# Kernel tuning notes

Hardware: AMD Instinct MI355X
Metric: run time of the kernel (lower is better)

Reference implementation:

```python
import jax, jax.numpy as jnp
import numpy as np

NEG_SLOPE = 0.2


def _gat_layer(x, src, dst, W, att_s, att_d, bias):
    # x: [N, F_in]; W: [F_in, H*C]; att_s/att_d: [H, C]; bias: [H*C]
    N = x.shape[0]
    H, C = att_s.shape
    h = (x @ W).reshape(N, H, C)                      # projected features [N,H,C]
    a_src = jnp.einsum('nhc,hc->nh', h, att_s)        # [N,H] per-node src logits
    a_dst = jnp.einsum('nhc,hc->nh', h, att_d)        # [N,H]
    e = a_src[src] + a_dst[dst]                       # [E,H] edge logits
    e = jnp.where(e > 0, e, NEG_SLOPE * e)            # leaky_relu
    # scatter-softmax over incoming edges of each destination node
    m = jax.ops.segment_max(e, dst, num_segments=N)   # [N,H]
    ex = jnp.exp(e - m[dst])                          # [E,H]
    denom = jax.ops.segment_sum(ex, dst, num_segments=N)  # [N,H]
    alpha = ex / denom[dst]                           # [E,H]
    # scatter-add aggregation of weighted source features
    msg = h[src] * alpha[:, :, None]                  # [E,H,C]
    out = jax.ops.segment_sum(msg, dst, num_segments=N)   # [N,H,C]
    return out.reshape(N, H * C) + bias


def _with_self_loops(edge_index, N):
    loop = jnp.arange(N, dtype=edge_index.dtype)
    src = jnp.concatenate([edge_index[0], loop])
    dst = jnp.concatenate([edge_index[1], loop])
    return src, dst


def setup_inputs() -> dict:
    key = jax.random.key(0)
    ks = jax.random.split(key, 10)
    N, E = 50000, 800000
    F_in, C1, H1, F_out = 128, 64, 4, 128
    x = jax.random.normal(ks[0], (N, F_in), dtype=jnp.float32)
    edge_index = jax.random.randint(ks[1], (2, E), 0, N, dtype=jnp.int64)
    s1 = 1.0 / np.sqrt(F_in)
    W1 = jax.random.normal(ks[2], (F_in, H1 * C1), dtype=jnp.float32) * s1
    att_src1 = jax.random.normal(ks[3], (H1, C1), dtype=jnp.float32) * 0.1
    att_dst1 = jax.random.normal(ks[4], (H1, C1), dtype=jnp.float32) * 0.1
    bias1 = jnp.zeros((H1 * C1,), dtype=jnp.float32)
    s2 = 1.0 / np.sqrt(H1 * C1)
    W2 = jax.random.normal(ks[5], (H1 * C1, F_out), dtype=jnp.float32) * s2
    att_src2 = jax.random.normal(ks[6], (1, F_out), dtype=jnp.float32) * 0.1
    att_dst2 = jax.random.normal(ks[7], (1, F_out), dtype=jnp.float32) * 0.1
    bias2 = jnp.zeros((F_out,), dtype=jnp.float32)
    return {"x": x, "edge_index": edge_index,
            "W1": W1, "att_src1": att_src1, "att_dst1": att_dst1, "bias1": bias1,
            "W2": W2, "att_src2": att_src2, "att_dst2": att_dst2, "bias2": bias2}


def reference(x, edge_index, W1, att_src1, att_dst1, bias1,
              W2, att_src2, att_dst2, bias2):
    N = x.shape[0]
    src, dst = _with_self_loops(edge_index, N)
    h1 = _gat_layer(x, src, dst, W1, att_src1, att_dst1, bias1)
    h1 = jax.nn.elu(h1)
    out = _gat_layer(h1, src, dst, W2, att_src2, att_dst2, bias2)
    return out
```

## Files before the change

kernel.cpp:

```cpp
#include <hip/hip_runtime.h>

#define NN 50000
#define NE 800000

constexpr int H1 = 4, F1 = 128, HC1 = 256;
constexpr int HC2 = 128;

typedef unsigned short u16;
typedef unsigned int u32;
typedef __attribute__((ext_vector_type(8))) short bf16x8;
typedef __attribute__((ext_vector_type(4))) float f32x4;

__device__ __forceinline__ float bf2f(u16 h) {
    return __uint_as_float(((u32)h) << 16);
}
__device__ __forceinline__ u16 f2bf(float f) {
    u32 u = __float_as_uint(f);
    u32 r = (u + 0x7fffu + ((u >> 16) & 1u)) >> 16;
    return (u16)r;
}

__device__ __forceinline__ int ld_edge(const int* e32, const long long* e64, int is64, long long idx) {
    return is64 ? (int)e64[idx] : e32[idx];
}

__global__ __launch_bounds__(256) void k_prep(
    const float* __restrict__ x, const float* __restrict__ W1, const float* __restrict__ W2,
    const float* __restrict__ as1w, const float* __restrict__ ad1w,
    const float* __restrict__ as2w, const float* __restrict__ ad2w,
    u16* __restrict__ xb, u16* __restrict__ wp1, u16* __restrict__ wp2,
    float* __restrict__ wa1, float* __restrict__ wa2)
{
    const int b = blockIdx.x, tid = threadIdx.x;
    if (b < 3125) {
        int i = b * 256 + tid;
        const float4* p = (const float4*)x + (size_t)i * 2;
        float4 a = p[0], c = p[1];
        ushort4 o0, o1;
        o0.x = f2bf(a.x); o0.y = f2bf(a.y); o0.z = f2bf(a.z); o0.w = f2bf(a.w);
        o1.x = f2bf(c.x); o1.y = f2bf(c.y); o1.z = f2bf(c.z); o1.w = f2bf(c.w);
        ((ushort4*)xb)[(size_t)i * 2] = o0;
        ((ushort4*)xb)[(size_t)i * 2 + 1] = o1;
    } else if (b < 3253) {
        int o = (b - 3125) * 256 + tid;
        int j = o & 7, lk = (o >> 3) & 3, nn = (o >> 5) & 255, kc = o >> 13;
        int k = kc * 32 + lk * 8 + j;
        wp1[o] = f2bf(W1[(size_t)k * HC1 + nn]);
    } else if (b < 3381) {
        int o = (b - 3253) * 256 + tid;
        int j = o & 7, lk = (o >> 3) & 3, nn = (o >> 5) & 127, kc = o >> 12;
        int k = kc * 32 + lk * 8 + j;
        wp2[o] = f2bf(W2[(size_t)k * HC2 + nn]);
    } else {
        #pragma unroll
        for (int pp = 0; pp < 2; pp++) {
            int p = tid + pp * 256;
            int k = p >> 2, h = p & 3;
            float s = 0.f, d = 0.f;
            for (int c = 0; c < 64; c++) {
                float wv = W1[(size_t)k * HC1 + h * 64 + c];
                s = fmaf(wv, as1w[h * 64 + c], s);
                d = fmaf(wv, ad1w[h * 64 + c], d);
            }
            wa1[h * 128 + k] = s;
            wa1[(4 + h) * 128 + k] = d;
        }
        {
            int k = tid;
            float s = 0.f, d = 0.f;
            for (int c = 0; c < 128; c++) {
                float wv = W2[(size_t)k * HC2 + c];
                s = fmaf(wv, as2w[c], s);
                d = fmaf(wv, ad2w[c], d);
            }
            wa2[k * 2] = s;
            wa2[k * 2 + 1] = d;
        }
    }
}

__global__ void k_zero_detect(int* __restrict__ p, const int* __restrict__ e32, int* __restrict__ flag) {
    int i = blockIdx.x * blockDim.x + threadIdx.x;
    if (i < NN) p[i] = 1;
    if (i == 0) {
        int z = 1;
        for (int t = 0; t < 16; t++)
            if (e32[2 * t + 1] != 0) z = 0;
        *flag = z;
    }
}

__global__ void k_count(const int* __restrict__ e32, const long long* __restrict__ e64,
                        const int* __restrict__ flag, int* __restrict__ deg) {
    int e = blockIdx.x * blockDim.x + threadIdx.x;
    if (e >= NE) return;
    int is64 = *flag;
    int dst = ld_edge(e32, e64, is64, (long long)NE + e);
    atomicAdd(&deg[dst], 1);
}

__global__ __launch_bounds__(256) void k_part(const int* __restrict__ deg, int* __restrict__ bsum) {
    int i = blockIdx.x * 256 + threadIdx.x;
    int v = (i < NN) ? deg[i] : 0;
    #pragma unroll
    for (int off = 1; off < 64; off <<= 1) v += __shfl_xor(v, off);
    __shared__ int ws[4];
    if ((threadIdx.x & 63) == 0) ws[threadIdx.x >> 6] = v;
    __syncthreads();
    if (threadIdx.x == 0) bsum[blockIdx.x] = ws[0] + ws[1] + ws[2] + ws[3];
}

__global__ __launch_bounds__(256) void k_scanb(const int* __restrict__ bsum, int* __restrict__ boff,
                                               int* __restrict__ row_ptr, int NB) {
    const int tid = threadIdx.x;
    const int lane = tid & 63, wv = tid >> 6;
    int v = (tid < NB) ? bsum[tid] : 0;
    int x = v;
    #pragma unroll
    for (int off = 1; off < 64; off <<= 1) {
        int t = __shfl_up(x, off);
        if (lane >= off) x += t;
    }
    __shared__ int wsum[4], woff[4];
    if (lane == 63) wsum[wv] = x;
    __syncthreads();
    if (tid == 0) {
        int run = 0;
        #pragma unroll
        for (int j = 0; j < 4; j++) { woff[j] = run; run += wsum[j]; }
        row_ptr[NN] = run;
    }
    __syncthreads();
    if (tid < NB) boff[tid] = x - v + woff[wv];
}

__global__ __launch_bounds__(256) void k_addb(const int* __restrict__ deg, const int* __restrict__ boff,
                                              int* __restrict__ row_ptr, int* __restrict__ cursor,
                                              int* __restrict__ col) {
    const int tid = threadIdx.x;
    const int lane = tid & 63, wv = tid >> 6;
    int i = blockIdx.x * 256 + tid;
    int v = (i < NN) ? deg[i] : 0;
    int x = v;
    #pragma unroll
    for (int off = 1; off < 64; off <<= 1) {
        int t = __shfl_up(x, off);
        if (lane >= off) x += t;
    }
    __shared__ int wsum[4], woff[4];
    if (lane == 63) wsum[wv] = x;
    __syncthreads();
    if (tid == 0) {
        int run = 0;
        #pragma unroll
        for (int j = 0; j < 4; j++) { woff[j] = run; run += wsum[j]; }
    }
    __syncthreads();
    int excl = x - v + woff[wv] + boff[blockIdx.x];
    if (i < NN) {
        row_ptr[i] = excl;
        cursor[i] = excl + 1;
        col[excl] = i;
    }
}

__global__ void k_fill(const int* __restrict__ e32, const long long* __restrict__ e64,
                       const int* __restrict__ flag, int* __restrict__ cursor, int* __restrict__ col) {
    int e = blockIdx.x * blockDim.x + threadIdx.x;
    if (e >= NE) return;
    int is64 = *flag;
    int src = ld_edge(e32, e64, is64, e);
    int dst = ld_edge(e32, e64, is64, (long long)NE + e);
    int pos = atomicAdd(&cursor[dst], 1);
    col[pos] = src;
}

template <int K, int NOUT, int TPB>
__global__ __launch_bounds__(TPB) void k_gemm_mfma(
    const u16* __restrict__ Ab, const u16* __restrict__ Wp, u16* __restrict__ Hout, int M)
{
    constexpr int BM = 64, BK = 32;
    constexpr int NK = K / BK;
    constexpr int LDA = 40;
    __shared__ __align__(16) u16 As[2][BM * LDA];

    const int tid = threadIdx.x;
    const int w = tid >> 6;
    const int l = tid & 63;
    const int l15 = l & 15, lk = l >> 4;
    const int row0 = blockIdx.x * BM;
    const int col0 = w * 64;

    f32x4 acc[4][4];
    #pragma unroll
    for (int rt = 0; rt < 4; rt++)
        #pragma unroll
        for (int nt = 0; nt < 4; nt++)
            acc[rt][nt] = (f32x4){0.f, 0.f, 0.f, 0.f};

    auto stage = [&](int kc, int b) {
        #pragma unroll
        for (int i = tid; i < BM * 4; i += TPB) {
            int r = i >> 2, c = (i & 3) * 8;
            int gr = row0 + r;
            bf16x8 v = {0, 0, 0, 0, 0, 0, 0, 0};
            if (gr < M) v = *(const bf16x8*)(Ab + (size_t)gr * K + kc * BK + c);
            *(bf16x8*)&As[b][r * LDA + c] = v;
        }
    };
    auto loadB = [&](int kc, bf16x8* bf) {
        #pragma unroll
        for (int nt = 0; nt < 4; nt++)
            bf[nt] = *(const bf16x8*)(Wp + (((size_t)kc * NOUT + col0 + nt * 16 + l15) * 4 + lk) * 8);
    };

    bf16x8 bcur[4];
    loadB(0, bcur);
    stage(0, 0);
    for (int kc = 0; kc < NK; ++kc) {
        __syncthreads();
        bf16x8 afr[4];
        #pragma unroll
        for (int rt = 0; rt < 4; rt++)
            afr[rt] = *(const bf16x8*)&As[kc & 1][(rt * 16 + l15) * LDA + lk * 8];
        bf16x8 bnext[4];
        if (kc + 1 < NK) {
            loadB(kc + 1, bnext);
            stage(kc + 1, (kc + 1) & 1);
        }
        #pragma unroll
        for (int rt = 0; rt < 4; rt++)
            #pragma unroll
            for (int nt = 0; nt < 4; nt++)
                acc[rt][nt] = __builtin_amdgcn_mfma_f32_16x16x32_bf16(afr[rt], bcur[nt], acc[rt][nt], 0, 0, 0);
        if (kc + 1 < NK) {
            #pragma unroll
            for (int nt = 0; nt < 4; nt++) bcur[nt] = bnext[nt];
        }
    }

    #pragma unroll
    for (int rt = 0; rt < 4; rt++) {
        #pragma unroll
        for (int t = 0; t < 4; t++) {
            int gr = row0 + rt * 16 + lk * 4 + t;
            if (gr < M) {
                #pragma unroll
                for (int nt = 0; nt < 4; nt++)
                    Hout[(size_t)gr * NOUT + col0 + nt * 16 + l15] = f2bf(acc[rt][nt][t]);
            }
        }
    }
}

__global__ __launch_bounds__(256) void k_logits1(
    const u16* __restrict__ xb, const float* __restrict__ wa1,
    float* __restrict__ as1, float* __restrict__ ad1)
{
    __shared__ float wsm[8 * 128];
    for (int i = threadIdx.x; i < 1024; i += 256) wsm[i] = wa1[i];
    __syncthreads();
    int n = blockIdx.x * 4 + (threadIdx.x >> 6);
    int l = threadIdx.x & 63;
    u32 xx = *(const u32*)(xb + (size_t)n * F1 + l * 2);
    float x0 = bf2f((u16)(xx & 0xffff)), x1 = bf2f((u16)(xx >> 16));
    float a[8];
    #pragma unroll
    for (int j = 0; j < 8; j++)
        a[j] = x0 * wsm[j * 128 + l * 2] + x1 * wsm[j * 128 + l * 2 + 1];
    #pragma unroll
    for (int off = 1; off < 64; off <<= 1) {
        #pragma unroll
        for (int j = 0; j < 8; j++) a[j] += __shfl_xor(a[j], off);
    }
    if (l == 0) {
        *(float4*)(as1 + (size_t)n * 4) = make_float4(a[0], a[1], a[2], a[3]);
        *(float4*)(ad1 + (size_t)n * 4) = make_float4(a[4], a[5], a[6], a[7]);
    }
}

__global__ __launch_bounds__(256) void k_agg1(
    const int* __restrict__ row_ptr, const int* __restrict__ col,
    const u16* __restrict__ Hb, const float* __restrict__ as_, const float* __restrict__ ad_,
    const float* __restrict__ bias, const float* __restrict__ wa2,
    u16* __restrict__ outp, float* __restrict__ as2, float* __restrict__ ad2)
{
    __shared__ int    s_src[4][64];
    __shared__ float4 s_p[4][64];
    int n = blockIdx.x * 4 + (threadIdx.x >> 6);
    const int lane = threadIdx.x & 63;
    const int wv = threadIdx.x >> 6;
    const int head = lane >> 4;
    float4 ad4 = *(const float4*)(ad_ + (size_t)n * 4);
    int beg = row_ptr[n];
    int cnt = row_ptr[n + 1] - beg;
    float4 sp = make_float4(0.f, 0.f, 0.f, 0.f);
    float ax = 0.f, ay = 0.f, az = 0.f, aw = 0.f;
    for (int c = 0; c < cnt; c += 64) {
        int idx = c + lane;
        int srcl = 0;
        float4 p4 = make_float4(0.f, 0.f, 0.f, 0.f);
        if (idx < cnt) {
            srcl = __builtin_nontemporal_load(col + beg + idx);
            float4 a4 = *(const float4*)(as_ + (size_t)srcl * 4);
            float e;
            e = a4.x + ad4.x; e = e > 0.f ? e : 0.2f * e; p4.x = __expf(e);
            e = a4.y + ad4.y; e = e > 0.f ? e : 0.2f * e; p4.y = __expf(e);
            e = a4.z + ad4.z; e = e > 0.f ? e : 0.2f * e; p4.z = __expf(e);
            e = a4.w + ad4.w; e = e > 0.f ? e : 0.2f * e; p4.w = __expf(e);
        }
        sp.x += p4.x; sp.y += p4.y; sp.z += p4.z; sp.w += p4.w;
        s_src[wv][lane] = srcl;
        s_p[wv][lane] = p4;
        int jmax = min(64, cnt - c);
        #pragma unroll 4
        for (int j = 0; j < jmax; ++j) {
            int srcj = s_src[wv][j];
            float pj = ((const float*)&s_p[wv][j])[head];
            ushort4 hv = *(const ushort4*)(Hb + (size_t)srcj * HC1 + lane * 4);
            ax = fmaf(pj, bf2f(hv.x), ax);
            ay = fmaf(pj, bf2f(hv.y), ay);
            az = fmaf(pj, bf2f(hv.z), az);
            aw = fmaf(pj, bf2f(hv.w), aw);
        }
    }
    #pragma unroll
    for (int off = 1; off < 64; off <<= 1) {
        sp.x += __shfl_xor(sp.x, off);
        sp.y += __shfl_xor(sp.y, off);
        sp.z += __shfl_xor(sp.z, off);
        sp.w += __shfl_xor(sp.w, off);
    }
    float s = head < 2 ? (head == 0 ? sp.x : sp.y) : (head == 2 ? sp.z : sp.w);
    float inv = 1.f / s;
    float4 bv = *(const float4*)(bias + lane * 4);
    float4 o;
    o.x = ax * inv + bv.x;
    o.y = ay * inv + bv.y;
    o.z = az * inv + bv.z;
    o.w = aw * inv + bv.w;
    o.x = o.x > 0.f ? o.x : __expf(o.x) - 1.f;
    o.y = o.y > 0.f ? o.y : __expf(o.y) - 1.f;
    o.z = o.z > 0.f ? o.z : __expf(o.z) - 1.f;
    o.w = o.w > 0.f ? o.w : __expf(o.w) - 1.f;
    ushort4 ob;
    ob.x = f2bf(o.x); ob.y = f2bf(o.y); ob.z = f2bf(o.z); ob.w = f2bf(o.w);
    *(ushort4*)(outp + (size_t)n * HC1 + lane * 4) = ob;

    float4 wA = *(const float4*)(wa2 + lane * 8);
    float4 wB = *(const float4*)(wa2 + lane * 8 + 4);
    float s2 = o.x * wA.x + o.y * wA.z + o.z * wB.x + o.w * wB.z;
    float d2 = o.x * wA.y + o.y * wA.w + o.z * wB.y + o.w * wB.w;
    #pragma unroll
    for (int off = 1; off < 64; off <<= 1) {
        s2 += __shfl_xor(s2, off);
        d2 += __shfl_xor(d2, off);
    }
    if (lane == 0) { as2[n] = s2; ad2[n] = d2; }
}

__global__ __launch_bounds__(256) void k_agg2(
    const int* __restrict__ row_ptr, const int* __restrict__ col,
    const u16* __restrict__ Hb, const float* __restrict__ as_, const float* __restrict__ ad_,
    const float* __restrict__ bias, float* __restrict__ outp)
{
    __shared__ int   s_src[4][64];
    __shared__ float s_p[4][64];
    int n = blockIdx.x * 4 + (threadIdx.x >> 6);
    const int lane = threadIdx.x & 63;
    const int wv = threadIdx.x >> 6;
    float ad0 = ad_[n];
    int beg = row_ptr[n];
    int cnt = row_ptr[n + 1] - beg;
    float sp = 0.f;
    float ax = 0.f, ay = 0.f;
    for (int c = 0; c < cnt; c += 64) {
        int idx = c + lane;
        int srcl = 0;
        float p = 0.f;
        if (idx < cnt) {
            srcl = __builtin_nontemporal_load(col + beg + idx);
            float e = as_[srcl] + ad0;
            e = e > 0.f ? e : 0.2f * e;
            p = __expf(e);
        }
        sp += p;
        s_src[wv][lane] = srcl;
        s_p[wv][lane] = p;
        int jmax = min(64, cnt - c);
        #pragma unroll 4
        for (int j = 0; j < jmax; ++j) {
            int srcj = s_src[wv][j];
            float pj = s_p[wv][j];
            ushort2 hv = *(const ushort2*)(Hb + (size_t)srcj * HC2 + lane * 2);
            ax = fmaf(pj, bf2f(hv.x), ax);
            ay = fmaf(pj, bf2f(hv.y), ay);
        }
    }
    #pragma unroll
    for (int off = 1; off < 64; off <<= 1) sp += __shfl_xor(sp, off);
    float inv = 1.f / sp;
    float2 bv = *(const float2*)(bias + lane * 2);
    float2 o = make_float2(ax * inv + bv.x, ay * inv + bv.y);
    *(float2*)(outp + (size_t)n * HC2 + lane * 2) = o;
}

extern "C" void kernel_launch(void* const* d_in, const int* in_sizes, int n_in,
                              void* d_out, int out_size, void* d_ws, size_t ws_size,
                              hipStream_t stream) {
    const float* x   = (const float*)d_in[0];
    const int*       e32 = (const int*)d_in[1];
    const long long* e64 = (const long long*)d_in[1];
    const float* W1  = (const float*)d_in[2];
    const float* as1w = (const float*)d_in[3];
    const float* ad1w = (const float*)d_in[4];
    const float* b1  = (const float*)d_in[5];
    const float* W2  = (const float*)d_in[6];
    const float* as2w = (const float*)d_in[7];
    const float* ad2w = (const float*)d_in[8];
    const float* b2  = (const float*)d_in[9];
    float* out = (float*)d_out;

    char* w = (char*)d_ws;
    auto carve = [&](size_t bytes) -> void* {
        void* p = (void*)w;
        w += (bytes + 255) & ~(size_t)255;
        return p;
    };
    int*   flag    = (int*)carve(4);
    int*   row_ptr = (int*)carve((NN + 1) * sizeof(int));
    int*   cursor  = (int*)carve(NN * sizeof(int));
    int*   col     = (int*)carve((NE + NN) * sizeof(int));
    int*   bsum    = (int*)carve(256 * sizeof(int));
    int*   boff    = (int*)carve(256 * sizeof(int));
    float* as1     = (float*)carve((size_t)NN * H1 * sizeof(float));
    float* ad1     = (float*)carve((size_t)NN * H1 * sizeof(float));
    float* as2     = (float*)carve((size_t)NN * sizeof(float));
    float* ad2     = (float*)carve((size_t)NN * sizeof(float));
    u16*   xb      = (u16*)carve((size_t)NN * F1 * sizeof(u16));
    u16*   h1b     = (u16*)carve((size_t)NN * HC1 * sizeof(u16));
    u16*   h2in    = (u16*)carve((size_t)NN * HC1 * sizeof(u16));
    u16*   h2b     = (u16*)carve((size_t)NN * HC2 * sizeof(u16));
    u16*   wp1     = (u16*)carve((size_t)F1 * HC1 * sizeof(u16));
    u16*   wp2     = (u16*)carve((size_t)HC1 * HC2 * sizeof(u16));
    float* wa1     = (float*)carve(8 * 128 * sizeof(float));
    float* wa2     = (float*)carve(256 * 2 * sizeof(float));

    const int TPB = 256;
    const int gN  = (NN + TPB - 1) / TPB;
    const int gE  = (NE + TPB - 1) / TPB;
    const int gM  = (NN + 63) / 64;
    const int gAgg = NN / 4;

    k_prep<<<3382, 256, 0, stream>>>(x, W1, W2, as1w, ad1w, as2w, ad2w, xb, wp1, wp2, wa1, wa2);

    k_zero_detect<<<gN, TPB, 0, stream>>>(cursor, e32, flag);
    k_count<<<gE, TPB, 0, stream>>>(e32, e64, flag, cursor);
    k_part<<<gN, TPB, 0, stream>>>(cursor, bsum);
    k_scanb<<<1, 256, 0, stream>>>(bsum, boff, row_ptr, gN);
    k_addb<<<gN, TPB, 0, stream>>>(cursor, boff, row_ptr, cursor, col);
    k_fill<<<gE, TPB, 0, stream>>>(e32, e64, flag, cursor, col);

    k_gemm_mfma<F1, HC1, 256><<<gM, 256, 0, stream>>>(xb, wp1, h1b, NN);
    k_logits1<<<gAgg, 256, 0, stream>>>(xb, wa1, as1, ad1);
    k_agg1<<<gAgg, TPB, 0, stream>>>(row_ptr, col, h1b, as1, ad1, b1, wa2, h2in, as2, ad2);

    k_gemm_mfma<HC1, HC2, 128><<<gM, 128, 0, stream>>>(h2in, wp2, h2b, NN);
    k_agg2<<<gAgg, TPB, 0, stream>>>(row_ptr, col, h2b, as2, ad2, b2, out);
}
```

Measured before the change: 276.0 us.

## Slice feature tables into 32-channel column blocks and split aggregation across slices

The GEMM now writes projected features in a sliced layout (32-channel slabs, node-major within each slab). Edge softmax weights are precomputed per edge into a buffer by a separate kernel, and aggregation is split into per-slice blocks. In each block, 8 lanes cover 32 channels and 8 edges are processed in parallel, then reduced with shuffles. The aim is to shrink the random-gather working set per block so it stays cache resident and to raise parallelism per destination node. The cost is extra kernel launches, an extra edge-weight buffer written and read, and col/row_ptr being reread once per slice.

```diff
diff --git a/kernel.cpp b/kernel.cpp
--- a/kernel.cpp
+++ b/kernel.cpp
@@ -2,6 +2,7 @@
 
 #define NN 50000
 #define NE 800000
+#define NEA (NE + NN)
 
 constexpr int H1 = 4, F1 = 128, HC1 = 256;
 constexpr int HC2 = 128;
@@ -246,8 +247,10 @@
             int gr = row0 + rt * 16 + lk * 4 + t;
             if (gr < M) {
                 #pragma unroll
-                for (int nt = 0; nt < 4; nt++)
-                    Hout[(size_t)gr * NOUT + col0 + nt * 16 + l15] = f2bf(acc[rt][nt][t]);
+                for (int nt = 0; nt < 4; nt++) {
+                    int c = col0 + nt * 16 + l15;
+                    Hout[((size_t)(c >> 5) * NN + gr) * 32 + (c & 31)] = f2bf(acc[rt][nt][t]);
+                }
             }
         }
     }
@@ -279,130 +282,155 @@
     }
 }
 
-__global__ __launch_bounds__(256) void k_agg1(
-    const int* __restrict__ row_ptr, const int* __restrict__ col,
-    const u16* __restrict__ Hb, const float* __restrict__ as_, const float* __restrict__ ad_,
-    const float* __restrict__ bias, const float* __restrict__ wa2,
-    u16* __restrict__ outp, float* __restrict__ as2, float* __restrict__ ad2)
+__global__ __launch_bounds__(256) void k_logits2(
+    const u16* __restrict__ h2in, const float* __restrict__ wa2,
+    float* __restrict__ as2, float* __restrict__ ad2)
 {
-    __shared__ int    s_src[4][64];
-    __shared__ float4 s_p[4][64];
     int n = blockIdx.x * 4 + (threadIdx.x >> 6);
-    const int lane = threadIdx.x & 63;
-    const int wv = threadIdx.x >> 6;
-    const int head = lane >> 4;
-    float4 ad4 = *(const float4*)(ad_ + (size_t)n * 4);
-    int beg = row_ptr[n];
-    int cnt = row_ptr[n + 1] - beg;
-    float4 sp = make_float4(0.f, 0.f, 0.f, 0.f);
-    float ax = 0.f, ay = 0.f, az = 0.f, aw = 0.f;
-    for (int c = 0; c < cnt; c += 64) {
-        int idx = c + lane;
-        int srcl = 0;
-        float4 p4 = make_float4(0.f, 0.f, 0.f, 0.f);
-        if (idx < cnt) {
-            srcl = __builtin_nontemporal_load(col + beg + idx);
-            float4 a4 = *(const float4*)(as_ + (size_t)srcl * 4);
-            float e;
-            e = a4.x + ad4.x; e = e > 0.f ? e : 0.2f * e; p4.x = __expf(e);
-            e = a4.y + ad4.y; e = e > 0.f ? e : 0.2f * e; p4.y = __expf(e);
-            e = a4.z + ad4.z; e = e > 0.f ? e : 0.2f * e; p4.z = __expf(e);
-            e = a4.w + ad4.w; e = e > 0.f ? e : 0.2f * e; p4.w = __expf(e);
-        }
-        sp.x += p4.x; sp.y += p4.y; sp.z += p4.z; sp.w += p4.w;
-        s_src[wv][lane] = srcl;
-        s_p[wv][lane] = p4;
-        int jmax = min(64, cnt - c);
-        #pragma unroll 4
-        for (int j = 0; j < jmax; ++j) {
-            int srcj = s_src[wv][j];
-            float pj = ((const float*)&s_p[wv][j])[head];
-            ushort4 hv = *(const ushort4*)(Hb + (size_t)srcj * HC1 + lane * 4);
-            ax = fmaf(pj, bf2f(hv.x), ax);
-            ay = fmaf(pj, bf2f(hv.y), ay);
-            az = fmaf(pj, bf2f(hv.z), az);
-            aw = fmaf(pj, bf2f(hv.w), aw);
-        }
-    }
-    #pragma unroll
-    for (int off = 1; off < 64; off <<= 1) {
-        sp.x += __shfl_xor(sp.x, off);
-        sp.y += __shfl_xor(sp.y, off);
-        sp.z += __shfl_xor(sp.z, off);
-        sp.w += __shfl_xor(sp.w, off);
-    }
-    float s = head < 2 ? (head == 0 ? sp.x : sp.y) : (head == 2 ? sp.z : sp.w);
-    float inv = 1.f / s;
-    float4 bv = *(const float4*)(bias + lane * 4);
-    float4 o;
-    o.x = ax * inv + bv.x;
-    o.y = ay * inv + bv.y;
-    o.z = az * inv + bv.z;
-    o.w = aw * inv + bv.w;
-    o.x = o.x > 0.f ? o.x : __expf(o.x) - 1.f;
-    o.y = o.y > 0.f ? o.y : __expf(o.y) - 1.f;
-    o.z = o.z > 0.f ? o.z : __expf(o.z) - 1.f;
-    o.w = o.w > 0.f ? o.w : __expf(o.w) - 1.f;
-    ushort4 ob;
-    ob.x = f2bf(o.x); ob.y = f2bf(o.y); ob.z = f2bf(o.z); ob.w = f2bf(o.w);
-    *(ushort4*)(outp + (size_t)n * HC1 + lane * 4) = ob;
-
-    float4 wA = *(const float4*)(wa2 + lane * 8);
-    float4 wB = *(const float4*)(wa2 + lane * 8 + 4);
-    float s2 = o.x * wA.x + o.y * wA.z + o.z * wB.x + o.w * wB.z;
-    float d2 = o.x * wA.y + o.y * wA.w + o.z * wB.y + o.w * wB.w;
+    int l = threadIdx.x & 63;
+    ushort4 hv = *(const ushort4*)(h2in + (size_t)n * HC1 + l * 4);
+    float4 wA = *(const float4*)(wa2 + l * 8);
+    float4 wB = *(const float4*)(wa2 + l * 8 + 4);
+    float h0 = bf2f(hv.x), h1 = bf2f(hv.y), h2 = bf2f(hv.z), h3 = bf2f(hv.w);
+    float s2 = h0 * wA.x + h1 * wA.z + h2 * wB.x + h3 * wB.z;
+    float d2 = h0 * wA.y + h1 * wA.w + h2 * wB.y + h3 * wB.w;
     #pragma unroll
     for (int off = 1; off < 64; off <<= 1) {
         s2 += __shfl_xor(s2, off);
         d2 += __shfl_xor(d2, off);
     }
-    if (lane == 0) { as2[n] = s2; ad2[n] = d2; }
-}
-
-__global__ __launch_bounds__(256) void k_agg2(
+    if (l == 0) { as2[n] = s2; ad2[n] = d2; }
+}
+
+template <int HEADS>
+__global__ __launch_bounds__(256) void k_edgep(
     const int* __restrict__ row_ptr, const int* __restrict__ col,
-    const u16* __restrict__ Hb, const float* __restrict__ as_, const float* __restrict__ ad_,
-    const float* __restrict__ bias, float* __restrict__ outp)
+    const float* __restrict__ as_, const float* __restrict__ ad_,
+    float* __restrict__ pb, float* __restrict__ inv)
+{
+    int n = blockIdx.x * 4 + (threadIdx.x >> 6);
+    const int lane = threadIdx.x & 63;
+    int beg = row_ptr[n];
+    int cnt = row_ptr[n + 1] - beg;
+    if (HEADS == 4) {
+        float4 ad4 = *(const float4*)(ad_ + (size_t)n * 4);
+        float4 sp = make_float4(0.f, 0.f, 0.f, 0.f);
+        for (int c = 0; c < cnt; c += 64) {
+            int idx = c + lane;
+            if (idx < cnt) {
+                int e = beg + idx;
+                int srcl = __builtin_nontemporal_load(col + e);
+                float4 a4 = *(const float4*)(as_ + (size_t)srcl * 4);
+                float t, p0, p1, p2, p3;
+                t = a4.x + ad4.x; t = t > 0.f ? t : 0.2f * t; p0 = __expf(t);
+                t = a4.y + ad4.y; t = t > 0.f ? t : 0.2f * t; p1 = __expf(t);
+                t = a4.z + ad4.z; t = t > 0.f ? t : 0.2f * t; p2 = __expf(t);
+                t = a4.w + ad4.w; t = t > 0.f ? t : 0.2f * t; p3 = __expf(t);
+                pb[e] = p0; pb[NEA + e] = p1; pb[2 * NEA + e] = p2; pb[3 * NEA + e] = p3;
+                sp.x += p0; sp.y += p1; sp.z += p2; sp.w += p3;
+            }
+        }
+        #pragma unroll
+        for (int off = 1; off < 64; off <<= 1) {
+            sp.x += __shfl_xor(sp.x, off);
+            sp.y += __shfl_xor(sp.y, off);
+            sp.z += __shfl_xor(sp.z, off);
+            sp.w += __shfl_xor(sp.w, off);
+        }
+        if (lane == 0)
+            *(float4*)(inv + (size_t)n * 4) =
+                make_float4(1.f / sp.x, 1.f / sp.y, 1.f / sp.z, 1.f / sp.w);
+    } else {
+        float ad0 = ad_[n];
+        float sp = 0.f;
+        for (int c = 0; c < cnt; c += 64) {
+            int idx = c + lane;
+            if (idx < cnt) {
+                int e = beg + idx;
+                int srcl = __builtin_nontemporal_load(col + e);
+                float t = as_[srcl] + ad0;
+                t = t > 0.f ? t : 0.2f * t;
+                float p = __expf(t);
+                pb[e] = p;
+                sp += p;
+            }
+        }
+        #pragma unroll
+        for (int off = 1; off < 64; off <<= 1) sp += __shfl_xor(sp, off);
+        if (lane == 0) inv[n] = 1.f / sp;
+    }
+}
+
+template <int NOUT, int NSLICE, int HEADS, int FINAL>
+__global__ __launch_bounds__(256) void k_aggs(
+    const int* __restrict__ row_ptr, const int* __restrict__ col, const u16* __restrict__ Hs,
+    const float* __restrict__ pb, const float* __restrict__ inv,
+    const float* __restrict__ bias, void* __restrict__ outp)
 {
     __shared__ int   s_src[4][64];
     __shared__ float s_p[4][64];
-    int n = blockIdx.x * 4 + (threadIdx.x >> 6);
-    const int lane = threadIdx.x & 63;
-    const int wv = threadIdx.x >> 6;
-    float ad0 = ad_[n];
+    const int b = blockIdx.x;
+    const int slice = b & (NSLICE - 1);
+    const int nb = b / NSLICE;
+    const int wv = threadIdx.x >> 6, lane = threadIdx.x & 63;
+    const int n = nb * 4 + wv;
+    const int head = (HEADS == 4) ? (slice >> 1) : 0;
+    const int sub = lane >> 3, l8 = lane & 7;
+    const u16* tab = Hs + (size_t)slice * NN * 32;
+    const float* pbs = pb + (size_t)head * NEA;
+
     int beg = row_ptr[n];
     int cnt = row_ptr[n + 1] - beg;
-    float sp = 0.f;
-    float ax = 0.f, ay = 0.f;
+    float a0 = 0.f, a1 = 0.f, a2 = 0.f, a3 = 0.f;
     for (int c = 0; c < cnt; c += 64) {
         int idx = c + lane;
         int srcl = 0;
         float p = 0.f;
         if (idx < cnt) {
             srcl = __builtin_nontemporal_load(col + beg + idx);
-            float e = as_[srcl] + ad0;
-            e = e > 0.f ? e : 0.2f * e;
-            p = __expf(e);
-        }
-        sp += p;
+            p = __builtin_nontemporal_load(pbs + beg + idx);
+        }
         s_src[wv][lane] = srcl;
         s_p[wv][lane] = p;
-        int jmax = min(64, cnt - c);
-        #pragma unroll 4
-        for (int j = 0; j < jmax; ++j) {
-            int srcj = s_src[wv][j];
-            float pj = s_p[wv][j];
-            ushort2 hv = *(const ushort2*)(Hb + (size_t)srcj * HC2 + lane * 2);
-            ax = fmaf(pj, bf2f(hv.x), ax);
-            ay = fmaf(pj, bf2f(hv.y), ay);
-        }
-    }
-    #pragma unroll
-    for (int off = 1; off < 64; off <<= 1) sp += __shfl_xor(sp, off);
-    float inv = 1.f / sp;
-    float2 bv = *(const float2*)(bias + lane * 2);
-    float2 o = make_float2(ax * inv + bv.x, ay * inv + bv.y);
-    *(float2*)(outp + (size_t)n * HC2 + lane * 2) = o;
+        int njit = (min(64, cnt - c) + 7) >> 3;
+        for (int j = 0; j < njit; ++j) {
+            int srcj = s_src[wv][j * 8 + sub];
+            float pj = s_p[wv][j * 8 + sub];
+            ushort4 hv = *(const ushort4*)(tab + (size_t)srcj * 32 + l8 * 4);
+            a0 = fmaf(pj, bf2f(hv.x), a0);
+            a1 = fmaf(pj, bf2f(hv.y), a1);
+            a2 = fmaf(pj, bf2f(hv.z), a2);
+            a3 = fmaf(pj, bf2f(hv.w), a3);
+        }
+    }
+    #pragma unroll
+    for (int off = 8; off <= 32; off <<= 1) {
+        a0 += __shfl_xor(a0, off);
+        a1 += __shfl_xor(a1, off);
+        a2 += __shfl_xor(a2, off);
+        a3 += __shfl_xor(a3, off);
+    }
+    if (lane < 8) {
+        float iv = inv[(size_t)n * HEADS + head];
+        int ch = slice * 32 + l8 * 4;
+        float4 bv = *(const float4*)(bias + ch);
+        float4 o;
+        o.x = a0 * iv + bv.x;
+        o.y = a1 * iv + bv.y;
+        o.z = a2 * iv + bv.z;
+        o.w = a3 * iv + bv.w;
+        if (FINAL) {
+            *(float4*)((float*)outp + (size_t)n * NOUT + ch) = o;
+        } else {
+            o.x = o.x > 0.f ? o.x : __expf(o.x) - 1.f;
+            o.y = o.y > 0.f ? o.y : __expf(o.y) - 1.f;
+            o.z = o.z > 0.f ? o.z : __expf(o.z) - 1.f;
+            o.w = o.w > 0.f ? o.w : __expf(o.w) - 1.f;
+            ushort4 ob;
+            ob.x = f2bf(o.x); ob.y = f2bf(o.y); ob.z = f2bf(o.z); ob.w = f2bf(o.w);
+            *(ushort4*)((u16*)outp + (size_t)n * NOUT + ch) = ob;
+        }
+    }
 }
 
 extern "C" void kernel_launch(void* const* d_in, const int* in_sizes, int n_in,
@@ -430,13 +458,16 @@
     int*   flag    = (int*)carve(4);
     int*   row_ptr = (int*)carve((NN + 1) * sizeof(int));
     int*   cursor  = (int*)carve(NN * sizeof(int));
-    int*   col     = (int*)carve((NE + NN) * sizeof(int));
+    int*   col     = (int*)carve((size_t)NEA * sizeof(int));
     int*   bsum    = (int*)carve(256 * sizeof(int));
     int*   boff    = (int*)carve(256 * sizeof(int));
     float* as1     = (float*)carve((size_t)NN * H1 * sizeof(float));
     float* ad1     = (float*)carve((size_t)NN * H1 * sizeof(float));
     float* as2     = (float*)carve((size_t)NN * sizeof(float));
     float* ad2     = (float*)carve((size_t)NN * sizeof(float));
+    float* inv1    = (float*)carve((size_t)NN * H1 * sizeof(float));
+    float* inv2    = (float*)carve((size_t)NN * sizeof(float));
+    float* pb      = (float*)carve((size_t)4 * NEA * sizeof(float));
     u16*   xb      = (u16*)carve((size_t)NN * F1 * sizeof(u16));
     u16*   h1b     = (u16*)carve((size_t)NN * HC1 * sizeof(u16));
     u16*   h2in    = (u16*)carve((size_t)NN * HC1 * sizeof(u16));
@@ -450,7 +481,7 @@
     const int gN  = (NN + TPB - 1) / TPB;
     const int gE  = (NE + TPB - 1) / TPB;
     const int gM  = (NN + 63) / 64;
-    const int gAgg = NN / 4;
+    const int gW  = NN / 4;
 
     k_prep<<<3382, 256, 0, stream>>>(x, W1, W2, as1w, ad1w, as2w, ad2w, xb, wp1, wp2, wa1, wa2);
 
@@ -462,9 +493,12 @@
     k_fill<<<gE, TPB, 0, stream>>>(e32, e64, flag, cursor, col);
 
     k_gemm_mfma<F1, HC1, 256><<<gM, 256, 0, stream>>>(xb, wp1, h1b, NN);
-    k_logits1<<<gAgg, 256, 0, stream>>>(xb, wa1, as1, ad1);
-    k_agg1<<<gAgg, TPB, 0, stream>>>(row_ptr, col, h1b, as1, ad1, b1, wa2, h2in, as2, ad2);
+    k_logits1<<<gW, 256, 0, stream>>>(xb, wa1, as1, ad1);
+    k_edgep<H1><<<gW, TPB, 0, stream>>>(row_ptr, col, as1, ad1, pb, inv1);
+    k_aggs<HC1, 8, H1, 0><<<gW * 8, TPB, 0, stream>>>(row_ptr, col, h1b, pb, inv1, b1, h2in);
 
     k_gemm_mfma<HC1, HC2, 128><<<gM, 128, 0, stream>>>(h2in, wp2, h2b, NN);
-    k_agg2<<<gAgg, TPB, 0, stream>>>(row_ptr, col, h2b, as2, ad2, b2, out);
-}
+    k_logits2<<<gW, 256, 0, stream>>>(h2in, wa2, as2, ad2);
+    k_edgep<1><<<gW, TPB, 0, stream>>>(row_ptr, col, as2, ad2, pb, inv2);
+    k_aggs<HC2, 4, 1, 1><<<gW * 4, TPB, 0, stream>>>(row_ptr, col, h2b, pb, inv2, b2, out);
+}
```

Result: slower. 460.9 us (+67.0%).
